# Kernel tuning notes

Measured on AMD Instinct MI355X. Metric: run time of the kernel, lower is better.

Reference implementation:

```python
import jax, jax.numpy as jnp
import numpy as np

N_POINTS = 2_000_000
IN_CH = 10
OUT_CH = 32  # out_channel // 2 for non-last layer
NUM_PILLARS = 100_000
BN_EPS = 1e-3


def setup_inputs() -> dict:
    key = jax.random.key(0)
    k1, k2, k3, k4 = jax.random.split(key, 4)
    inputs = jax.random.normal(k1, (N_POINTS, IN_CH), dtype=jnp.float32)
    unq_inv = jax.random.randint(k2, (N_POINTS,), 0, NUM_PILLARS, dtype=jnp.int32)
    # Linear params (PyTorch nn.Linear: y = x @ W.T + b)
    W = jax.random.normal(k3, (OUT_CH, IN_CH), dtype=jnp.float32) * (1.0 / np.sqrt(IN_CH))
    b = jax.random.normal(k4, (OUT_CH,), dtype=jnp.float32) * 0.01
    # BatchNorm1d affine params
    gamma = jnp.ones((OUT_CH,), dtype=jnp.float32)
    beta = jnp.zeros((OUT_CH,), dtype=jnp.float32)
    return {"inputs": inputs, "W": W, "b": b, "gamma": gamma, "beta": beta,
            "unq_inv": unq_inv, "num_pillars": NUM_PILLARS}


def reference(inputs, W, b, gamma, beta, unq_inv, num_pillars):
    # Linear: [N, in] -> [N, out]
    v = inputs @ W.T + b
    # BatchNorm1d (training-mode batch stats, biased variance, eps=1e-3)
    mean = jnp.mean(v, axis=0)
    var = jnp.mean(jnp.square(v - mean), axis=0)
    xn = (v - mean) * jax.lax.rsqrt(var + BN_EPS) * gamma + beta
    x = jax.nn.relu(xn)
    # scatter_max over pillars (segment max along dim 0)
    x_max = jax.ops.segment_max(x, unq_inv, num_segments=num_pillars)  # [P, out]
    # gather back per point and average with per-point features
    return (x + x_max[unq_inv]) * 0.5
```

## Files before the change

### kernel.cpp

```cpp
#include <hip/hip_runtime.h>

#define NPTS    2000000
#define PIL     100000
#define BN_EPS_F 1e-3f

#define SHIFT   5
#define PPB     32
#define NBKT    3125
#define NBAC    256
#define CHUNK   7813
#define TILE    64
#define TDW     (TILE * 12)

#define ACC_OFF    0
#define WP_OFF     128
#define BP_OFF     512
#define PART_OFF   1024
#define TOTS_OFF   17920
#define STARTS_OFF 21248
#define HIST_OFF   24576
#define PS_OFF     839680

__device__ __forceinline__ constexpr int tri_idx(int j, int k) {
    return j * 10 - j * (j - 1) / 2 + (k - j);
}

__global__ __launch_bounds__(512) void kA_hist(const int* __restrict__ unq,
                                               unsigned* __restrict__ hist)
{
    __shared__ unsigned h[NBKT];
    for (int i = threadIdx.x; i < NBKT; i += 512) h[i] = 0u;
    __syncthreads();
    const int lo = blockIdx.x * CHUNK;
    const int hi = min(lo + CHUNK, NPTS);
    for (int t = lo + threadIdx.x; t < hi; t += 512)
        atomicAdd(&h[unq[t] >> SHIFT], 1u);
    __syncthreads();
    for (int i = threadIdx.x; i < NBKT; i += 512)
        hist[(size_t)blockIdx.x * NBKT + i] = h[i];
}

__global__ __launch_bounds__(64) void kB1_colsum(const unsigned* __restrict__ hist,
                                                 unsigned* __restrict__ tots)
{
    const int c = blockIdx.x, lane = threadIdx.x;
    unsigned s = 0;
#pragma unroll
    for (int i = 0; i < NBAC / 64; ++i) s += hist[(size_t)(i * 64 + lane) * NBKT + c];
#pragma unroll
    for (int sh = 1; sh < 64; sh <<= 1) s += __shfl_xor(s, sh, 64);
    if (lane == 0) tots[c] = s;
}

__global__ __launch_bounds__(1024) void kB2_scan(const unsigned* __restrict__ tots,
                                                 unsigned* __restrict__ starts)
{
    __shared__ unsigned ps[1024];
    const int t = threadIdx.x;
    unsigned v[4], sum = 0;
#pragma unroll
    for (int i = 0; i < 4; ++i) {
        int idx = t * 4 + i;
        v[i] = (idx < NBKT) ? tots[idx] : 0u;
        sum += v[i];
    }
    ps[t] = sum;
    __syncthreads();
    for (int d = 1; d < 1024; d <<= 1) {
        unsigned x = (t >= d) ? ps[t - d] : 0u;
        __syncthreads();
        ps[t] += x;
        __syncthreads();
    }
    unsigned excl = ps[t] - sum;
#pragma unroll
    for (int i = 0; i < 4; ++i) {
        int idx = t * 4 + i;
        if (idx < NBKT) starts[idx] = excl;
        excl += v[i];
    }
    if (t == 1023) starts[NBKT] = ps[1023];
}

__global__ __launch_bounds__(64) void kB3_expand(unsigned* __restrict__ hist,
                                                 const unsigned* __restrict__ starts)
{
    const int c = blockIdx.x, lane = threadIdx.x;
    unsigned hv[NBAC / 64];
    unsigned psum = 0;
#pragma unroll
    for (int i = 0; i < NBAC / 64; ++i) {
        hv[i] = hist[(size_t)(lane * (NBAC / 64) + i) * NBKT + c];
        psum += hv[i];
    }
    unsigned incl = psum;
#pragma unroll
    for (int s = 1; s < 64; s <<= 1) {
        unsigned v = __shfl_up(incl, s, 64);
        if (lane >= s) incl += v;
    }
    unsigned run = starts[c] + (incl - psum);
#pragma unroll
    for (int i = 0; i < NBAC / 64; ++i) {
        hist[(size_t)(lane * (NBAC / 64) + i) * NBKT + c] = run;
        run += hv[i];
    }
}

__global__ __launch_bounds__(512) void kC2_scatter_mom(const float* __restrict__ in,
                                                       const int* __restrict__ unq,
                                                       const unsigned* __restrict__ off,
                                                       float4* __restrict__ ps4,
                                                       float* __restrict__ partial)
{
    __shared__ unsigned cur[NBKT];
    __shared__ float lds2[8][66];
    for (int i = threadIdx.x; i < NBKT; i += 512)
        cur[i] = off[(size_t)blockIdx.x * NBKT + i];
    __syncthreads();

    float acc[65];
#pragma unroll
    for (int i = 0; i < 65; ++i) acc[i] = 0.f;

    const int lo = blockIdx.x * CHUNK;
    const int hi = min(lo + CHUNK, NPTS);
    for (int t = lo + threadIdx.x; t < hi; t += 512) {
        int pil = unq[t];
        unsigned slot = atomicAdd(&cur[pil >> SHIFT], 1u);
        const float* px = in + (size_t)t * 10;
        float4 r0 = *reinterpret_cast<const float4*>(px);
        float4 r1 = *reinterpret_cast<const float4*>(px + 4);
        float2 r2 = *reinterpret_cast<const float2*>(px + 8);
        unsigned meta = ((unsigned)(pil & (PPB - 1)) << 21) | (unsigned)t;
        float4* d = ps4 + (size_t)slot * 3;
        d[0] = r0;
        d[1] = r1;
        d[2] = make_float4(r2.x, r2.y, __uint_as_float(meta), 0.f);

        float xf[10] = { r0.x, r0.y, r0.z, r0.w, r1.x, r1.y, r1.z, r1.w, r2.x, r2.y };
#pragma unroll
        for (int j = 0; j < 10; ++j) acc[j] += xf[j];
        int o = 10;
#pragma unroll
        for (int j = 0; j < 10; ++j)
#pragma unroll
            for (int k = j; k < 10; ++k) acc[o++] += xf[j] * xf[k];
    }

#pragma unroll
    for (int i = 0; i < 65; ++i) {
        float v = acc[i];
#pragma unroll
        for (int s = 1; s < 64; s <<= 1) v += __shfl_xor(v, s, 64);
        acc[i] = v;
    }
    const int wid = threadIdx.x >> 6, lane = threadIdx.x & 63;
    if (lane == 0) {
#pragma unroll
        for (int i = 0; i < 65; ++i) lds2[wid][i] = acc[i];
    }
    __syncthreads();
    if (threadIdx.x < 65) {
        float s = 0.f;
#pragma unroll
        for (int wv = 0; wv < 8; ++wv) s += lds2[wv][threadIdx.x];
        partial[(size_t)threadIdx.x * NBAC + blockIdx.x] = s;
    }
}

__global__ void k1_final(const float* __restrict__ partial, float* __restrict__ accum)
{
    const int e = blockIdx.x, lane = threadIdx.x;
    float s = 0.f;
#pragma unroll
    for (int i = 0; i < NBAC / 64; ++i) s += partial[(size_t)e * NBAC + i * 64 + lane];
#pragma unroll
    for (int sh = 1; sh < 64; sh <<= 1) s += __shfl_xor(s, sh, 64);
    if (lane == 0) accum[e] = s;
}

__global__ void k2_finalize(const float* __restrict__ accum, const float* __restrict__ W,
                            const float* __restrict__ b, const float* __restrict__ gamma,
                            const float* __restrict__ beta, float* __restrict__ Wp,
                            float* __restrict__ bp)
{
    int c = threadIdx.x;
    if (c >= 32) return;
    const float invN = 1.0f / (float)NPTS;
    float m[10], w[10];
#pragma unroll
    for (int k = 0; k < 10; ++k) m[k] = accum[k] * invN;
#pragma unroll
    for (int k = 0; k < 10; ++k) w[k] = W[c*10 + k];
    float mean = b[c];
#pragma unroll
    for (int k = 0; k < 10; ++k) mean += w[k] * m[k];
    float var = 0.f;
#pragma unroll
    for (int j = 0; j < 10; ++j) {
#pragma unroll
        for (int k = j; k < 10; ++k) {
            float Cjk = accum[10 + tri_idx(j, k)] * invN - m[j] * m[k];
            var += w[j] * w[k] * Cjk * ((j == k) ? 1.f : 2.f);
        }
    }
    float scale = gamma[c] * rsqrtf(var + BN_EPS_F);
#pragma unroll
    for (int k = 0; k < 10; ++k) Wp[c*10 + k] = w[k] * scale;
    bp[c] = (b[c] - mean) * scale + beta[c];
}

__device__ __forceinline__ float kd_affine(const float4& v0, const float4& v1,
                                           const float4& v2, const float* w, float bc)
{
    float a = bc;
    a += v0.x * w[0]; a += v0.y * w[1]; a += v0.z * w[2]; a += v0.w * w[3];
    a += v1.x * w[4]; a += v1.y * w[5]; a += v1.z * w[6]; a += v1.w * w[7];
    a += v2.x * w[8]; a += v2.y * w[9];
    return fmaxf(a, 0.f);
}

__global__ __launch_bounds__(256) void kD7_reduce(const float* __restrict__ psf,
                                                  const unsigned* __restrict__ starts,
                                                  const float* __restrict__ Wp,
                                                  const float* __restrict__ bp,
                                                  float* __restrict__ out)
{
    __shared__ unsigned tab[PPB * 32];
    __shared__ float sbuf[2][TDW];
    for (int i = threadIdx.x; i < PPB * 32; i += 256) tab[i] = 0u;

    const int c   = threadIdx.x & 31;
    const int sub = threadIdx.x >> 5;
    float w[10];
#pragma unroll
    for (int k = 0; k < 10; ++k) w[k] = Wp[c * 10 + k];
    const float bc = bp[c];

    const unsigned s0 = starts[blockIdx.x];
    const unsigned s1 = starts[blockIdx.x + 1];
    const unsigned nrec = s1 - s0;
    const int nch = (int)((nrec + TILE - 1) / TILE);
    const size_t gbase  = (size_t)s0 * 12;
    const size_t gend   = (size_t)NPTS * 12;

    float st[3];
    if (nch > 0) {
        size_t cb = gbase;
        if (cb + TDW <= gend) {
#pragma unroll
            for (int j = 0; j < 3; ++j) st[j] = psf[cb + threadIdx.x + j * 256];
        } else {
#pragma unroll
            for (int j = 0; j < 3; ++j) {
                size_t gi = cb + threadIdx.x + j * 256;
                st[j] = psf[gi < gend ? gi : gend - 1];
            }
        }
#pragma unroll
        for (int j = 0; j < 3; ++j) sbuf[0][threadIdx.x + j * 256] = st[j];
    }
    __syncthreads();

    for (int ci = 0; ci < nch; ++ci) {
        const bool more = (ci + 1 < nch);
        if (more) {
            size_t cb = gbase + (size_t)(ci + 1) * TDW;
            if (cb + TDW <= gend) {
#pragma unroll
                for (int j = 0; j < 3; ++j) st[j] = psf[cb + threadIdx.x + j * 256];
            } else {
#pragma unroll
                for (int j = 0; j < 3; ++j) {
                    size_t gi = cb + threadIdx.x + j * 256;
                    st[j] = psf[gi < gend ? gi : gend - 1];
                }
            }
        }
        const float4* s4 = reinterpret_cast<const float4*>(sbuf[ci & 1]);
        int rem = (int)nrec - ci * TILE;
        int rmax = rem < TILE ? rem : TILE;
        for (int r = sub; r < rmax; r += 8) {
            float4 v0 = s4[r * 3], v1 = s4[r * 3 + 1], v2 = s4[r * 3 + 2];
            unsigned meta = __float_as_uint(v2.z);
            unsigned pl = (meta >> 21) & (PPB - 1);
            float a = kd_affine(v0, v1, v2, w, bc);
            atomicMax(&tab[(pl << 5) + c], __float_as_uint(a));
        }
        __syncthreads();
        if (more) {
#pragma unroll
            for (int j = 0; j < 3; ++j) sbuf[(ci + 1) & 1][threadIdx.x + j * 256] = st[j];
        }
        __syncthreads();
    }

    if (nch > 0) {
        size_t cb = gbase;
        if (cb + TDW <= gend) {
#pragma unroll
            for (int j = 0; j < 3; ++j) st[j] = psf[cb + threadIdx.x + j * 256];
        } else {
#pragma unroll
            for (int j = 0; j < 3; ++j) {
                size_t gi = cb + threadIdx.x + j * 256;
                st[j] = psf[gi < gend ? gi : gend - 1];
            }
        }
#pragma unroll
        for (int j = 0; j < 3; ++j) sbuf[0][threadIdx.x + j * 256] = st[j];
    }
    __syncthreads();

    for (int ci = 0; ci < nch; ++ci) {
        const bool more = (ci + 1 < nch);
        if (more) {
            size_t cb = gbase + (size_t)(ci + 1) * TDW;
            if (cb + TDW <= gend) {
#pragma unroll
                for (int j = 0; j < 3; ++j) st[j] = psf[cb + threadIdx.x + j * 256];
            } else {
#pragma unroll
                for (int j = 0; j < 3; ++j) {
                    size_t gi = cb + threadIdx.x + j * 256;
                    st[j] = psf[gi < gend ? gi : gend - 1];
                }
            }
        }
        const float4* s4 = reinterpret_cast<const float4*>(sbuf[ci & 1]);
        int rem = (int)nrec - ci * TILE;
        int rmax = rem < TILE ? rem : TILE;
        for (int r = sub; r < rmax; r += 8) {
            float4 v0 = s4[r * 3], v1 = s4[r * 3 + 1], v2 = s4[r * 3 + 2];
            unsigned meta = __float_as_uint(v2.z);
            unsigned idx = meta & 0x1FFFFFu;
            unsigned pl = (meta >> 21) & (PPB - 1);
            float a = kd_affine(v0, v1, v2, w, bc);
            float mx = __uint_as_float(tab[(pl << 5) + c]);
            __builtin_nontemporal_store((a + mx) * 0.5f, &out[(size_t)idx * 32 + c]);
        }
        __syncthreads();
        if (more) {
#pragma unroll
            for (int j = 0; j < 3; ++j) sbuf[(ci + 1) & 1][threadIdx.x + j * 256] = st[j];
        }
        __syncthreads();
    }
}

extern "C" void kernel_launch(void* const* d_in, const int* in_sizes, int n_in,
                              void* d_out, int out_size, void* d_ws, size_t ws_size,
                              hipStream_t stream)
{
    const float* in    = (const float*)d_in[0];
    const float* W     = (const float*)d_in[1];
    const float* b     = (const float*)d_in[2];
    const float* gamma = (const float*)d_in[3];
    const float* beta  = (const float*)d_in[4];
    const int*   unq   = (const int*)d_in[5];

    float* ws      = (float*)d_ws;
    float* accum   = ws + ACC_OFF;
    float* Wp      = ws + WP_OFF;
    float* bp      = ws + BP_OFF;
    float* partial = ws + PART_OFF;
    unsigned* tots   = (unsigned*)(ws + TOTS_OFF);
    unsigned* starts = (unsigned*)(ws + STARTS_OFF);
    unsigned* hist   = (unsigned*)(ws + HIST_OFF);
    float4*   ps4    = (float4*)(ws + PS_OFF);

    kA_hist<<<NBAC, 512, 0, stream>>>(unq, hist);
    kB1_colsum<<<NBKT, 64, 0, stream>>>(hist, tots);
    kB2_scan<<<1, 1024, 0, stream>>>(tots, starts);
    kB3_expand<<<NBKT, 64, 0, stream>>>(hist, starts);
    kC2_scatter_mom<<<NBAC, 512, 0, stream>>>(in, unq, hist, ps4, partial);
    k1_final<<<65, 64, 0, stream>>>(partial, accum);
    k2_finalize<<<1, 64, 0, stream>>>(accum, W, b, gamma, beta, Wp, bp);
    kD7_reduce<<<NBKT, 256, 0, stream>>>((const float*)ps4, starts, Wp, bp, (float*)d_out);
}
```

Baseline: 187.4 us.

## Split pillar max and output write into separate kernels with coalesced output stores

```diff
diff --git a/kernel.cpp b/kernel.cpp
--- a/kernel.cpp
+++ b/kernel.cpp
@@ -20,6 +20,7 @@
 #define STARTS_OFF 21248
 #define HIST_OFF   24576
 #define PS_OFF     839680
+#define XMAX_OFF   24839680
 
 __device__ __forceinline__ constexpr int tri_idx(int j, int k) {
     return j * 10 - j * (j - 1) / 2 + (k - j);
@@ -221,11 +222,11 @@
     return fmaxf(a, 0.f);
 }
 
-__global__ __launch_bounds__(256) void kD7_reduce(const float* __restrict__ psf,
-                                                  const unsigned* __restrict__ starts,
-                                                  const float* __restrict__ Wp,
-                                                  const float* __restrict__ bp,
-                                                  float* __restrict__ out)
+__global__ __launch_bounds__(256) void kD9_max(const float* __restrict__ psf,
+                                               const unsigned* __restrict__ starts,
+                                               const float* __restrict__ Wp,
+                                               const float* __restrict__ bp,
+                                               float* __restrict__ xmax)
 {
     __shared__ unsigned tab[PPB * 32];
     __shared__ float sbuf[2][TDW];
@@ -296,56 +297,71 @@
         __syncthreads();
     }
 
-    if (nch > 0) {
-        size_t cb = gbase;
-        if (cb + TDW <= gend) {
-#pragma unroll
-            for (int j = 0; j < 3; ++j) st[j] = psf[cb + threadIdx.x + j * 256];
-        } else {
-#pragma unroll
-            for (int j = 0; j < 3; ++j) {
-                size_t gi = cb + threadIdx.x + j * 256;
-                st[j] = psf[gi < gend ? gi : gend - 1];
-            }
-        }
-#pragma unroll
-        for (int j = 0; j < 3; ++j) sbuf[0][threadIdx.x + j * 256] = st[j];
-    }
-    __syncthreads();
-
-    for (int ci = 0; ci < nch; ++ci) {
-        const bool more = (ci + 1 < nch);
-        if (more) {
-            size_t cb = gbase + (size_t)(ci + 1) * TDW;
-            if (cb + TDW <= gend) {
-#pragma unroll
-                for (int j = 0; j < 3; ++j) st[j] = psf[cb + threadIdx.x + j * 256];
-            } else {
-#pragma unroll
-                for (int j = 0; j < 3; ++j) {
-                    size_t gi = cb + threadIdx.x + j * 256;
-                    st[j] = psf[gi < gend ? gi : gend - 1];
-                }
-            }
-        }
-        const float4* s4 = reinterpret_cast<const float4*>(sbuf[ci & 1]);
-        int rem = (int)nrec - ci * TILE;
-        int rmax = rem < TILE ? rem : TILE;
-        for (int r = sub; r < rmax; r += 8) {
-            float4 v0 = s4[r * 3], v1 = s4[r * 3 + 1], v2 = s4[r * 3 + 2];
-            unsigned meta = __float_as_uint(v2.z);
-            unsigned idx = meta & 0x1FFFFFu;
-            unsigned pl = (meta >> 21) & (PPB - 1);
-            float a = kd_affine(v0, v1, v2, w, bc);
-            float mx = __uint_as_float(tab[(pl << 5) + c]);
-            __builtin_nontemporal_store((a + mx) * 0.5f, &out[(size_t)idx * 32 + c]);
-        }
-        __syncthreads();
-        if (more) {
-#pragma unroll
-            for (int j = 0; j < 3; ++j) sbuf[(ci + 1) & 1][threadIdx.x + j * 256] = st[j];
-        }
-        __syncthreads();
+    const size_t xbase = (size_t)blockIdx.x * (PPB * 32);
+#pragma unroll
+    for (int i = 0; i < (PPB * 32) / 256; ++i)
+        xmax[xbase + i * 256 + threadIdx.x] = __uint_as_float(tab[i * 256 + threadIdx.x]);
+}
+
+__global__ __launch_bounds__(256) void kE_out(const float* __restrict__ in,
+                                              const int* __restrict__ unq,
+                                              const float* __restrict__ xmax,
+                                              const float* __restrict__ Wp,
+                                              const float* __restrict__ bp,
+                                              float* __restrict__ out)
+{
+    const int c = threadIdx.x & 31;
+    float w[10];
+#pragma unroll
+    for (int k = 0; k < 10; ++k) w[k] = Wp[c * 10 + k];
+    const float bc = bp[c];
+
+    const int hw   = (blockIdx.x * 256 + threadIdx.x) >> 5;
+    const int step = (2048 * 256) >> 5;
+
+    int p = hw;
+    for (; p + step < NPTS; p += 2 * step) {
+        const int pA = p, pB = p + step;
+        const float* pxA = in + (size_t)pA * 10;
+        const float* pxB = in + (size_t)pB * 10;
+        float4 a0 = *reinterpret_cast<const float4*>(pxA);
+        float4 a1 = *reinterpret_cast<const float4*>(pxA + 4);
+        float2 a2 = *reinterpret_cast<const float2*>(pxA + 8);
+        float4 b0 = *reinterpret_cast<const float4*>(pxB);
+        float4 b1 = *reinterpret_cast<const float4*>(pxB + 4);
+        float2 b2 = *reinterpret_cast<const float2*>(pxB + 8);
+        int pilA = unq[pA];
+        int pilB = unq[pB];
+        float mxA = xmax[(size_t)pilA * 32 + c];
+        float mxB = xmax[(size_t)pilB * 32 + c];
+
+        float aA = bc;
+        aA += a0.x*w[0]; aA += a0.y*w[1]; aA += a0.z*w[2]; aA += a0.w*w[3];
+        aA += a1.x*w[4]; aA += a1.y*w[5]; aA += a1.z*w[6]; aA += a1.w*w[7];
+        aA += a2.x*w[8]; aA += a2.y*w[9];
+        aA = fmaxf(aA, 0.f);
+        float aB = bc;
+        aB += b0.x*w[0]; aB += b0.y*w[1]; aB += b0.z*w[2]; aB += b0.w*w[3];
+        aB += b1.x*w[4]; aB += b1.y*w[5]; aB += b1.z*w[6]; aB += b1.w*w[7];
+        aB += b2.x*w[8]; aB += b2.y*w[9];
+        aB = fmaxf(aB, 0.f);
+
+        __builtin_nontemporal_store((aA + mxA) * 0.5f, &out[(size_t)pA * 32 + c]);
+        __builtin_nontemporal_store((aB + mxB) * 0.5f, &out[(size_t)pB * 32 + c]);
+    }
+    for (; p < NPTS; p += step) {
+        const float* px = in + (size_t)p * 10;
+        float4 v0 = *reinterpret_cast<const float4*>(px);
+        float4 v1 = *reinterpret_cast<const float4*>(px + 4);
+        float2 v2 = *reinterpret_cast<const float2*>(px + 8);
+        int pil = unq[p];
+        float mx = xmax[(size_t)pil * 32 + c];
+        float a = bc;
+        a += v0.x*w[0]; a += v0.y*w[1]; a += v0.z*w[2]; a += v0.w*w[3];
+        a += v1.x*w[4]; a += v1.y*w[5]; a += v1.z*w[6]; a += v1.w*w[7];
+        a += v2.x*w[8]; a += v2.y*w[9];
+        a = fmaxf(a, 0.f);
+        __builtin_nontemporal_store((a + mx) * 0.5f, &out[(size_t)p * 32 + c]);
     }
 }
 
@@ -369,6 +385,7 @@
     unsigned* starts = (unsigned*)(ws + STARTS_OFF);
     unsigned* hist   = (unsigned*)(ws + HIST_OFF);
     float4*   ps4    = (float4*)(ws + PS_OFF);
+    float*    xmax   = ws + XMAX_OFF;
 
     kA_hist<<<NBAC, 512, 0, stream>>>(unq, hist);
     kB1_colsum<<<NBKT, 64, 0, stream>>>(hist, tots);
@@ -377,5 +394,6 @@
     kC2_scatter_mom<<<NBAC, 512, 0, stream>>>(in, unq, hist, ps4, partial);
     k1_final<<<65, 64, 0, stream>>>(partial, accum);
     k2_finalize<<<1, 64, 0, stream>>>(accum, W, b, gamma, beta, Wp, bp);
-    kD7_reduce<<<NBKT, 256, 0, stream>>>((const float*)ps4, starts, Wp, bp, (float*)d_out);
-}
+    kD9_max<<<NBKT, 256, 0, stream>>>((const float*)ps4, starts, Wp, bp, xmax);
+    kE_out<<<2048, 256, 0, stream>>>(in, unq, xmax, Wp, bp, (float*)d_out);
+}
```

After: 259.3 us. +38.4%, slower.
